# Optimization experiments

Hardware: AMD Instinct MI355X
Metric: run time of the kernel (lower is better)

The kernel has to match this reference:

```python
import jax, jax.numpy as jnp
import numpy as np

N = 100000
E = 1600000
IN_C = 512
OUT_C = 128


def setup_inputs() -> dict:
    key = jax.random.key(0)
    k1, k2, k3, k4 = jax.random.split(key, 4)
    x = jax.random.normal(k1, (N, IN_C), dtype=jnp.float32)
    edge_index = jax.random.randint(k2, (2, E), 0, N, dtype=jnp.int64)
    # GCNConv parameters (glorot weight, zero bias as in PyG defaults)
    scale = jnp.sqrt(6.0 / (IN_C + OUT_C)).astype(jnp.float32)
    W = jax.random.uniform(k3, (IN_C, OUT_C), dtype=jnp.float32, minval=-scale, maxval=scale)
    b = jnp.zeros((OUT_C,), dtype=jnp.float32)
    return {"x": x, "edge_index": edge_index, "W": W, "b": b}


def reference(x, edge_index, W, b):
    n = x.shape[0]
    loops = jnp.arange(n, dtype=edge_index.dtype)
    src = jnp.concatenate([edge_index[0], loops])  # [E+N] message sources
    dst = jnp.concatenate([edge_index[1], loops])  # [E+N] message targets
    # symmetric GCN normalization: deg over targets incl. self-loops
    deg = jax.ops.segment_sum(jnp.ones_like(src, dtype=x.dtype), dst, num_segments=n)
    dinv = jnp.where(deg > 0, jax.lax.rsqrt(deg), 0.0)
    norm = dinv[src] * dinv[dst]  # [E+N]
    h = x @ W  # [N, OUT_C] transform first (in > out)
    msg = h[src] * norm[:, None]  # [E+N, OUT_C]
    out = jax.ops.segment_sum(msg, dst, num_segments=n) + b
    return (out, 0)
```

## Files before the change

### kernel.cpp

```cpp
#include <hip/hip_runtime.h>

#define IN_C 512
#define OUT_C 128
#define NB 128
#define CHUNK 8192

typedef float f32x4 __attribute__((ext_vector_type(4)));
typedef __bf16 bf16x8 __attribute__((ext_vector_type(8)));

static inline int cdiv(int a, int b) { return (a + b - 1) / b; }

__device__ __forceinline__ unsigned short bfbits(__bf16 h) {
  return __builtin_bit_cast(unsigned short, h);
}


__global__ __launch_bounds__(256) void hist_kernel(const int* __restrict__ dst,
                                                   int* __restrict__ table,
                                                   const float* __restrict__ W,
                                                   unsigned short* __restrict__ wfh,
                                                   unsigned short* __restrict__ wfl,
                                                   int nchunks, int E) {
  int c = blockIdx.x;
  int t = threadIdx.x;
  if (c >= nchunks) {
    int i = (c - nchunks) * 256 + t;
    if (i < IN_C * OUT_C) {
      int k = i >> 7;
      int col = i & 127;
      float w = W[i];
      __bf16 hb = (__bf16)w;
      __bf16 lb = (__bf16)(w - (float)hb);
      int ks = k >> 5;
      int lg = (k & 31) >> 3;
      int j = k & 7;
      int cb = col >> 4;
      int lane = lg * 16 + (col & 15);
      size_t idx = ((size_t)(ks * 8 + cb) * 64 + lane) * 8 + j;
      wfh[idx] = bfbits(hb);
      wfl[idx] = bfbits(lb);
    }
    return;
  }
  __shared__ int hcnt[NB];
  if (t < NB) hcnt[t] = 0;
  __syncthreads();
  int base = c * CHUNK;
  int lim = base + CHUNK < E ? base + CHUNK : E;
  for (int e = base + t; e < lim; e += 256) {
    atomicAdd(&hcnt[dst[e] >> 10], 1);
  }
  __syncthreads();
  if (t < NB) table[t * nchunks + c] = hcnt[t];
}

__global__ __launch_bounds__(256) void tscan_kernel(int* __restrict__ table,
                                                    int* __restrict__ bstart,
                                                    int nchunks, int E) {
  __shared__ int sh[256];
  int t = threadIdx.x;
  int total = NB * nchunks;
  int S = (total + 255) / 256;
  int lo = t * S;
  int hi = lo + S; if (hi > total) hi = total;
  int s = 0;
  int i = lo;
  for (; i + 4 <= hi; i += 4)
    s += table[i] + table[i + 1] + table[i + 2] + table[i + 3];
  for (; i < hi; i++) s += table[i];
  sh[t] = s;
  __syncthreads();
  for (int off = 1; off < 256; off <<= 1) {
    int x = sh[t];
    if (t >= off) x += sh[t - off];
    __syncthreads();
    sh[t] = x;
    __syncthreads();
  }
  int run = sh[t] - s;
  for (i = lo; i < hi; i++) {
    int v = table[i];
    table[i] = run;
    run += v;
  }
  __syncthreads();
  for (int b = t; b < NB; b += 256) bstart[b] = table[b * nchunks];
  if (t == 0) bstart[NB] = E;
}

__global__ __launch_bounds__(256) void scat2_kernel(const int* __restrict__ src,
                                                    const int* __restrict__ dst,
                                                    const int* __restrict__ table,
                                                    int* __restrict__ inter,
                                                    int nchunks, int E) {
  __shared__ int cur[NB];
  int t = threadIdx.x;
  int c = blockIdx.x;
  if (t < NB) cur[t] = table[t * nchunks + c];
  __syncthreads();
  int base = c * CHUNK;
  int lim = base + CHUNK < E ? base + CHUNK : E;
  for (int e = base + t; e < lim; e += 256) {
    int d = dst[e];
    int pos = atomicAdd(&cur[d >> 10], 1);
    inter[pos] = (src[e] << 10) | (d & 1023);
  }
}

__global__ __launch_bounds__(256) void bucket_csr_kernel(const int* __restrict__ inter,
                                                         const int* __restrict__ bstart,
                                                         int* __restrict__ offs,
                                                         float* __restrict__ dinv,
                                                         int* __restrict__ csr_src,
                                                         int n, int E, int nbk) {
  __shared__ int dl[1024];
  __shared__ int curs[1024];
  __shared__ int sh[256];
  int t = threadIdx.x;
  int b = blockIdx.x;
  for (int i = t; i < 1024; i += 256) dl[i] = 0;
  __syncthreads();
  int lo = bstart[b], hi = bstart[b + 1];
  for (int e = lo + t; e < hi; e += 256) atomicAdd(&dl[inter[e] & 1023], 1);
  __syncthreads();
  int c[4];
  int s = 0;
#pragma unroll
  for (int j = 0; j < 4; j++) {
    c[j] = dl[t * 4 + j];
    s += c[j];
  }
  sh[t] = s;
  __syncthreads();
  for (int off = 1; off < 256; off <<= 1) {
    int x = sh[t];
    if (t >= off) x += sh[t - off];
    __syncthreads();
    sh[t] = x;
    __syncthreads();
  }
  int run = sh[t] - s + lo;
  int nb0 = b << 10;
#pragma unroll
  for (int j = 0; j < 4; j++) {
    int node = nb0 + t * 4 + j;
    if (node < n) {
      offs[node] = run;
      dinv[node] = rsqrtf((float)c[j] + 1.0f);
    }
    curs[t * 4 + j] = run;
    run += c[j];
  }
  if (b == nbk - 1 && t == 255) offs[n] = E;
  __syncthreads();
  for (int e = lo + t; e < hi; e += 256) {
    int u = inter[e];
    int pos = atomicAdd(&curs[u & 1023], 1);
    csr_src[pos] = u >> 10;
  }
}

__global__ __launch_bounds__(256) void gemm_mfma_kernel(
    const float* __restrict__ x, const unsigned short* __restrict__ wfh,
    const unsigned short* __restrict__ wfl, const float* __restrict__ dinv,
    unsigned short* __restrict__ h, int n) {
  __shared__ float xs[2][4096];

  const int tid = threadIdx.x;
  const int wv = tid >> 6;
  const int lane = tid & 63;
  const int l15 = lane & 15;
  const int lg = lane >> 4;
  const int wr = wv >> 1;
  const int wc = wv & 1;
  const int row0 = blockIdx.x * 128;

  const float* gsrc[4];
#pragma unroll
  for (int i = 0; i < 4; i++) {
    int pslot = i * 256 + tid;
    int row = pslot >> 3;
    int q = pslot & 7;
    int s = q ^ (row & 7);
    int grow = row0 + row;
    if (grow > n - 1) grow = n - 1;
    gsrc[i] = x + (size_t)grow * IN_C + s * 4;
  }

  const unsigned short* bph = wfh + ((size_t)(wc * 4) * 64 + lane) * 8;
  const unsigned short* bpl = wfl + ((size_t)(wc * 4) * 64 + lane) * 8;

  f32x4 acc[4][4];
#pragma unroll
  for (int i = 0; i < 4; i++)
#pragma unroll
    for (int j = 0; j < 4; j++) acc[i][j] = (f32x4)0.0f;

#pragma unroll
  for (int i = 0; i < 4; i++) {
    char* lp = (char*)&xs[0][0] + i * 4096 + wv * 1024;
    __builtin_amdgcn_global_load_lds(
        (const __attribute__((address_space(1))) void*)gsrc[i],
        (__attribute__((address_space(3))) void*)lp, 16, 0, 0);
    gsrc[i] += 32;
  }
  __syncthreads();

  int cur = 0;
  for (int ks = 0; ks < 16; ks++) {
    if (ks < 15) {
#pragma unroll
      for (int i = 0; i < 4; i++) {
        char* lp = (char*)&xs[cur ^ 1][0] + i * 4096 + wv * 1024;
        __builtin_amdgcn_global_load_lds(
            (const __attribute__((address_space(1))) void*)gsrc[i],
            (__attribute__((address_space(3))) void*)lp, 16, 0, 0);
        gsrc[i] += 32;
      }
    }
    bf16x8 bh[4], bl[4];
#pragma unroll
    for (int nt = 0; nt < 4; nt++) {
      bh[nt] = __builtin_bit_cast(bf16x8, *(const uint4*)(bph + (size_t)ks * 4096 + nt * 512));
      bl[nt] = __builtin_bit_cast(bf16x8, *(const uint4*)(bpl + (size_t)ks * 4096 + nt * 512));
    }
    const float* bp = &xs[cur][0];
    bf16x8 ah[4];
#pragma unroll
    for (int rt = 0; rt < 4; rt++) {
      int row = wr * 64 + rt * 16 + l15;
      int r7 = row & 7;
      int s0 = (lg * 2) ^ r7;
      int s1 = (lg * 2 + 1) ^ r7;
      float4 f0 = *(const float4*)(bp + row * 32 + s0 * 4);
      float4 f1 = *(const float4*)(bp + row * 32 + s1 * 4);
      float f[8] = {f0.x, f0.y, f0.z, f0.w, f1.x, f1.y, f1.z, f1.w};
      bf16x8 hh;
#pragma unroll
      for (int j = 0; j < 8; j++) hh[j] = (__bf16)f[j];
      ah[rt] = hh;
    }
#pragma unroll
    for (int rt = 0; rt < 4; rt++)
#pragma unroll
      for (int nt = 0; nt < 4; nt++) {
        acc[rt][nt] = __builtin_amdgcn_mfma_f32_16x16x32_bf16(ah[rt], bh[nt], acc[rt][nt], 0, 0, 0);
        acc[rt][nt] = __builtin_amdgcn_mfma_f32_16x16x32_bf16(ah[rt], bl[nt], acc[rt][nt], 0, 0, 0);
      }
    __syncthreads();
    cur ^= 1;
  }

#pragma unroll
  for (int rt = 0; rt < 4; rt++) {
    int rowbase = row0 + wr * 64 + rt * 16 + lg * 4;
#pragma unroll
    for (int r = 0; r < 4; r++) {
      int row = rowbase + r;
      if (row < n) {
        float di = dinv[row];
#pragma unroll
        for (int nt = 0; nt < 4; nt++) {
          int col = wc * 64 + nt * 16 + l15;
          h[(size_t)row * OUT_C + col] = bfbits((__bf16)(acc[rt][nt][r] * di));
        }
      }
    }
  }
}

__device__ __forceinline__ float bflo(unsigned int u) {
  return __builtin_bit_cast(float, u << 16);
}
__device__ __forceinline__ float bfhi(unsigned int u) {
  return __builtin_bit_cast(float, u & 0xffff0000u);
}

__global__ __launch_bounds__(256) void gather_kernel(const int* __restrict__ offs,
                                                     const int* __restrict__ csr_src,
                                                     const unsigned short* __restrict__ h,
                                                     const float* __restrict__ dinv,
                                                     const float* __restrict__ b,
                                                     float* __restrict__ out,
                                                     int n, int tail) {
  int wid = threadIdx.x >> 6;
  int lane = threadIdx.x & 63;
  int l15 = lane & 15;
  int q = lane >> 4;
  int node = blockIdx.x * 4 + wid;
  if (node >= n) return;

  int start = offs[node];
  int end = offs[node + 1];

  float ax0 = 0, ay0 = 0, ax1 = 0, ay1 = 0, ax2 = 0, ay2 = 0, ax3 = 0, ay3 = 0;

  int e = start + q;
  for (; e + 12 < end; e += 16) {
    int s0 = csr_src[e];
    int s1 = csr_src[e + 4];
    int s2 = csr_src[e + 8];
    int s3 = csr_src[e + 12];
    uint4 u0 = *(const uint4*)(h + (size_t)s0 * OUT_C + l15 * 8);
    uint4 u1 = *(const uint4*)(h + (size_t)s1 * OUT_C + l15 * 8);
    uint4 u2 = *(const uint4*)(h + (size_t)s2 * OUT_C + l15 * 8);
    uint4 u3 = *(const uint4*)(h + (size_t)s3 * OUT_C + l15 * 8);
    ax0 += (bflo(u0.x) + bflo(u1.x)) + (bflo(u2.x) + bflo(u3.x));
    ay0 += (bfhi(u0.x) + bfhi(u1.x)) + (bfhi(u2.x) + bfhi(u3.x));
    ax1 += (bflo(u0.y) + bflo(u1.y)) + (bflo(u2.y) + bflo(u3.y));
    ay1 += (bfhi(u0.y) + bfhi(u1.y)) + (bfhi(u2.y) + bfhi(u3.y));
    ax2 += (bflo(u0.z) + bflo(u1.z)) + (bflo(u2.z) + bflo(u3.z));
    ay2 += (bfhi(u0.z) + bfhi(u1.z)) + (bfhi(u2.z) + bfhi(u3.z));
    ax3 += (bflo(u0.w) + bflo(u1.w)) + (bflo(u2.w) + bflo(u3.w));
    ay3 += (bfhi(u0.w) + bfhi(u1.w)) + (bfhi(u2.w) + bfhi(u3.w));
  }
  for (; e < end; e += 4) {
    int s0 = csr_src[e];
    uint4 u0 = *(const uint4*)(h + (size_t)s0 * OUT_C + l15 * 8);
    ax0 += bflo(u0.x); ay0 += bfhi(u0.x);
    ax1 += bflo(u0.y); ay1 += bfhi(u0.y);
    ax2 += bflo(u0.z); ay2 += bfhi(u0.z);
    ax3 += bflo(u0.w); ay3 += bfhi(u0.w);
  }

#pragma unroll
  for (int mask = 16; mask <= 32; mask <<= 1) {
    ax0 += __shfl_xor(ax0, mask); ay0 += __shfl_xor(ay0, mask);
    ax1 += __shfl_xor(ax1, mask); ay1 += __shfl_xor(ay1, mask);
    ax2 += __shfl_xor(ax2, mask); ay2 += __shfl_xor(ay2, mask);
    ax3 += __shfl_xor(ax3, mask); ay3 += __shfl_xor(ay3, mask);
  }

  float dd = dinv[node];
  uint4 us = *(const uint4*)(h + (size_t)node * OUT_C + l15 * 8);
  ax0 = (ax0 + bflo(us.x)) * dd; ay0 = (ay0 + bfhi(us.x)) * dd;
  ax1 = (ax1 + bflo(us.y)) * dd; ay1 = (ay1 + bfhi(us.y)) * dd;
  ax2 = (ax2 + bflo(us.z)) * dd; ay2 = (ay2 + bfhi(us.z)) * dd;
  ax3 = (ax3 + bflo(us.w)) * dd; ay3 = (ay3 + bfhi(us.w)) * dd;

  if (q == 0) {
    float4 b0 = *(const float4*)(b + l15 * 8);
    float4 b1 = *(const float4*)(b + l15 * 8 + 4);
    float4 o0 = make_float4(ax0 + b0.x, ay0 + b0.y, ax1 + b0.z, ay1 + b0.w);
    float4 o1 = make_float4(ax2 + b1.x, ay2 + b1.y, ax3 + b1.z, ay3 + b1.w);
    float* op = out + (size_t)node * OUT_C + l15 * 8;
    *(float4*)op = o0;
    *(float4*)(op + 4) = o1;
  }

  if (node == 0 && lane == 0) {
    for (int t = 0; t < tail; t++) out[(size_t)n * OUT_C + t] = 0.0f;
  }
}

extern "C" void kernel_launch(void* const* d_in, const int* in_sizes, int n_in,
                              void* d_out, int out_size, void* d_ws, size_t ws_size,
                              hipStream_t stream) {
  const float* x = (const float*)d_in[0];
  const int* ei = (const int*)d_in[1];
  const float* W = (const float*)d_in[2];
  const float* b = (const float*)d_in[3];

  const int n = in_sizes[0] / IN_C;
  const int E = in_sizes[1] / 2;
  const int* src = ei;
  const int* dst = ei + E;
  float* out = (float*)d_out;

  const int nchunks = cdiv(E, CHUNK);
  const int nbk = cdiv(n, 1024);

  size_t p = 0;
  auto alloc = [&](size_t bytes) { size_t o = p; p += (bytes + 255) & ~(size_t)255; return o; };
  char* ws = (char*)d_ws;
  float*          dinv   = (float*)(ws + alloc((size_t)n * 4));
  int*            offs   = (int*)(ws + alloc(((size_t)n + 1) * 4));
  int*            csrsrc = (int*)(ws + alloc((size_t)E * 4));
  int*            bstart = (int*)(ws + alloc((NB + 1) * 4));
  unsigned short* wfh    = (unsigned short*)(ws + alloc((size_t)IN_C * OUT_C * 2));
  unsigned short* wfl    = (unsigned short*)(ws + alloc((size_t)IN_C * OUT_C * 2));
  size_t upos = p;
  int*            inter  = (int*)(ws + upos);
  int*            table  = (int*)(ws + upos + (((size_t)E * 4 + 255) & ~(size_t)255));
  unsigned short* h      = (unsigned short*)(ws + upos);

  hist_kernel<<<nchunks + 256, 256, 0, stream>>>(dst, table, W, wfh, wfl, nchunks, E);
  tscan_kernel<<<1, 256, 0, stream>>>(table, bstart, nchunks, E);
  scat2_kernel<<<nchunks, 256, 0, stream>>>(src, dst, table, inter, nchunks, E);
  bucket_csr_kernel<<<nbk, 256, 0, stream>>>(inter, bstart, offs, dinv, csrsrc, n, E, nbk);
  gemm_mfma_kernel<<<cdiv(n, 128), 256, 0, stream>>>(x, wfh, wfl, dinv, h, n);
  int tail = out_size - n * OUT_C;
  gather_kernel<<<cdiv(n, 4), 256, 0, stream>>>(offs, csrsrc, h, dinv, b, out, n, tail);
}
```

Before: 257.6 us.

## Overlap GEMM tiles with CSR-building kernels and rescale h separately

```diff
diff --git a/kernel.cpp b/kernel.cpp
--- a/kernel.cpp
+++ b/kernel.cpp
@@ -13,7 +13,12 @@
 __device__ __forceinline__ unsigned short bfbits(__bf16 h) {
   return __builtin_bit_cast(unsigned short, h);
 }
-
+__device__ __forceinline__ float bflo(unsigned int u) {
+  return __builtin_bit_cast(float, u << 16);
+}
+__device__ __forceinline__ float bfhi(unsigned int u) {
+  return __builtin_bit_cast(float, u & 0xffff0000u);
+}
 
 __global__ __launch_bounds__(256) void hist_kernel(const int* __restrict__ dst,
                                                    int* __restrict__ table,
@@ -54,9 +59,123 @@
   if (t < NB) table[t * nchunks + c] = hcnt[t];
 }
 
-__global__ __launch_bounds__(256) void tscan_kernel(int* __restrict__ table,
-                                                    int* __restrict__ bstart,
-                                                    int nchunks, int E) {
+__device__ __forceinline__ void gemm_tile(
+    const float* __restrict__ x, const unsigned short* __restrict__ wfh,
+    const unsigned short* __restrict__ wfl, unsigned short* __restrict__ h,
+    int n, int tile) {
+  __shared__ float xs[2][4096];
+
+  const int tid = threadIdx.x;
+  const int wv = tid >> 6;
+  const int lane = tid & 63;
+  const int l15 = lane & 15;
+  const int lg = lane >> 4;
+  const int wr = wv >> 1;
+  const int wc = wv & 1;
+  const int row0 = tile * 128;
+
+  const float* gsrc[4];
+#pragma unroll
+  for (int i = 0; i < 4; i++) {
+    int pslot = i * 256 + tid;
+    int row = pslot >> 3;
+    int q = pslot & 7;
+    int s = q ^ (row & 7);
+    int grow = row0 + row;
+    if (grow > n - 1) grow = n - 1;
+    gsrc[i] = x + (size_t)grow * IN_C + s * 4;
+  }
+
+  const unsigned short* bph = wfh + ((size_t)(wc * 4) * 64 + lane) * 8;
+  const unsigned short* bpl = wfl + ((size_t)(wc * 4) * 64 + lane) * 8;
+
+  f32x4 acc[4][4];
+#pragma unroll
+  for (int i = 0; i < 4; i++)
+#pragma unroll
+    for (int j = 0; j < 4; j++) acc[i][j] = (f32x4)0.0f;
+
+#pragma unroll
+  for (int i = 0; i < 4; i++) {
+    char* lp = (char*)&xs[0][0] + i * 4096 + wv * 1024;
+    __builtin_amdgcn_global_load_lds(
+        (const __attribute__((address_space(1))) void*)gsrc[i],
+        (__attribute__((address_space(3))) void*)lp, 16, 0, 0);
+    gsrc[i] += 32;
+  }
+  __syncthreads();
+
+  int cur = 0;
+  for (int ks = 0; ks < 16; ks++) {
+    if (ks < 15) {
+#pragma unroll
+      for (int i = 0; i < 4; i++) {
+        char* lp = (char*)&xs[cur ^ 1][0] + i * 4096 + wv * 1024;
+        __builtin_amdgcn_global_load_lds(
+            (const __attribute__((address_space(1))) void*)gsrc[i],
+            (__attribute__((address_space(3))) void*)lp, 16, 0, 0);
+        gsrc[i] += 32;
+      }
+    }
+    bf16x8 bh[4], bl[4];
+#pragma unroll
+    for (int nt = 0; nt < 4; nt++) {
+      bh[nt] = __builtin_bit_cast(bf16x8, *(const uint4*)(bph + (size_t)ks * 4096 + nt * 512));
+      bl[nt] = __builtin_bit_cast(bf16x8, *(const uint4*)(bpl + (size_t)ks * 4096 + nt * 512));
+    }
+    const float* bp = &xs[cur][0];
+    bf16x8 ah[4];
+#pragma unroll
+    for (int rt = 0; rt < 4; rt++) {
+      int row = wr * 64 + rt * 16 + l15;
+      int r7 = row & 7;
+      int s0 = (lg * 2) ^ r7;
+      int s1 = (lg * 2 + 1) ^ r7;
+      float4 f0 = *(const float4*)(bp + row * 32 + s0 * 4);
+      float4 f1 = *(const float4*)(bp + row * 32 + s1 * 4);
+      float f[8] = {f0.x, f0.y, f0.z, f0.w, f1.x, f1.y, f1.z, f1.w};
+      bf16x8 hh;
+#pragma unroll
+      for (int j = 0; j < 8; j++) hh[j] = (__bf16)f[j];
+      ah[rt] = hh;
+    }
+#pragma unroll
+    for (int rt = 0; rt < 4; rt++)
+#pragma unroll
+      for (int nt = 0; nt < 4; nt++) {
+        acc[rt][nt] = __builtin_amdgcn_mfma_f32_16x16x32_bf16(ah[rt], bh[nt], acc[rt][nt], 0, 0, 0);
+        acc[rt][nt] = __builtin_amdgcn_mfma_f32_16x16x32_bf16(ah[rt], bl[nt], acc[rt][nt], 0, 0, 0);
+      }
+    __syncthreads();
+    cur ^= 1;
+  }
+
+#pragma unroll
+  for (int rt = 0; rt < 4; rt++) {
+    int rowbase = row0 + wr * 64 + rt * 16 + lg * 4;
+#pragma unroll
+    for (int r = 0; r < 4; r++) {
+      int row = rowbase + r;
+      if (row < n) {
+#pragma unroll
+        for (int nt = 0; nt < 4; nt++) {
+          int col = wc * 64 + nt * 16 + l15;
+          h[(size_t)row * OUT_C + col] = bfbits((__bf16)acc[rt][nt][r]);
+        }
+      }
+    }
+  }
+}
+
+__global__ __launch_bounds__(256) void tscan_gemm_kernel(
+    int* __restrict__ table, int* __restrict__ bstart,
+    const float* __restrict__ x, const unsigned short* __restrict__ wfh,
+    const unsigned short* __restrict__ wfl, unsigned short* __restrict__ h,
+    int nchunks, int E, int n, int tbase) {
+  if (blockIdx.x != 0) {
+    gemm_tile(x, wfh, wfl, h, n, tbase + (int)blockIdx.x - 1);
+    return;
+  }
   __shared__ int sh[256];
   int t = threadIdx.x;
   int total = NB * nchunks;
@@ -71,10 +190,10 @@
   sh[t] = s;
   __syncthreads();
   for (int off = 1; off < 256; off <<= 1) {
-    int x = sh[t];
-    if (t >= off) x += sh[t - off];
+    int x2 = sh[t];
+    if (t >= off) x2 += sh[t - off];
     __syncthreads();
-    sh[t] = x;
+    sh[t] = x2;
     __syncthreads();
   }
   int run = sh[t] - s;
@@ -88,11 +207,16 @@
   if (t == 0) bstart[NB] = E;
 }
 
-__global__ __launch_bounds__(256) void scat2_kernel(const int* __restrict__ src,
-                                                    const int* __restrict__ dst,
-                                                    const int* __restrict__ table,
-                                                    int* __restrict__ inter,
-                                                    int nchunks, int E) {
+__global__ __launch_bounds__(256) void scat2_gemm_kernel(
+    const int* __restrict__ src, const int* __restrict__ dst,
+    const int* __restrict__ table, int* __restrict__ inter,
+    const float* __restrict__ x, const unsigned short* __restrict__ wfh,
+    const unsigned short* __restrict__ wfl, unsigned short* __restrict__ h,
+    int nchunks, int E, int n, int tbase) {
+  if ((int)blockIdx.x >= nchunks) {
+    gemm_tile(x, wfh, wfl, h, n, tbase + (int)blockIdx.x - nchunks);
+    return;
+  }
   __shared__ int cur[NB];
   int t = threadIdx.x;
   int c = blockIdx.x;
@@ -107,12 +231,16 @@
   }
 }
 
-__global__ __launch_bounds__(256) void bucket_csr_kernel(const int* __restrict__ inter,
-                                                         const int* __restrict__ bstart,
-                                                         int* __restrict__ offs,
-                                                         float* __restrict__ dinv,
-                                                         int* __restrict__ csr_src,
-                                                         int n, int E, int nbk) {
+__global__ __launch_bounds__(256) void bucket_gemm_kernel(
+    const int* __restrict__ inter, const int* __restrict__ bstart,
+    int* __restrict__ offs, float* __restrict__ dinv, int* __restrict__ csr_src,
+    const float* __restrict__ x, const unsigned short* __restrict__ wfh,
+    const unsigned short* __restrict__ wfl, unsigned short* __restrict__ h,
+    int n, int E, int nbk, int tbase) {
+  if ((int)blockIdx.x >= nbk) {
+    gemm_tile(x, wfh, wfl, h, n, tbase + (int)blockIdx.x - nbk);
+    return;
+  }
   __shared__ int dl[1024];
   __shared__ int curs[1024];
   __shared__ int sh[256];
@@ -133,10 +261,10 @@
   sh[t] = s;
   __syncthreads();
   for (int off = 1; off < 256; off <<= 1) {
-    int x = sh[t];
-    if (t >= off) x += sh[t - off];
+    int x2 = sh[t];
+    if (t >= off) x2 += sh[t - off];
     __syncthreads();
-    sh[t] = x;
+    sh[t] = x2;
     __syncthreads();
   }
   int run = sh[t] - s + lo;
@@ -160,120 +288,22 @@
   }
 }
 
-__global__ __launch_bounds__(256) void gemm_mfma_kernel(
-    const float* __restrict__ x, const unsigned short* __restrict__ wfh,
-    const unsigned short* __restrict__ wfl, const float* __restrict__ dinv,
-    unsigned short* __restrict__ h, int n) {
-  __shared__ float xs[2][4096];
-
-  const int tid = threadIdx.x;
-  const int wv = tid >> 6;
-  const int lane = tid & 63;
-  const int l15 = lane & 15;
-  const int lg = lane >> 4;
-  const int wr = wv >> 1;
-  const int wc = wv & 1;
-  const int row0 = blockIdx.x * 128;
-
-  const float* gsrc[4];
-#pragma unroll
-  for (int i = 0; i < 4; i++) {
-    int pslot = i * 256 + tid;
-    int row = pslot >> 3;
-    int q = pslot & 7;
-    int s = q ^ (row & 7);
-    int grow = row0 + row;
-    if (grow > n - 1) grow = n - 1;
-    gsrc[i] = x + (size_t)grow * IN_C + s * 4;
-  }
-
-  const unsigned short* bph = wfh + ((size_t)(wc * 4) * 64 + lane) * 8;
-  const unsigned short* bpl = wfl + ((size_t)(wc * 4) * 64 + lane) * 8;
-
-  f32x4 acc[4][4];
-#pragma unroll
-  for (int i = 0; i < 4; i++)
-#pragma unroll
-    for (int j = 0; j < 4; j++) acc[i][j] = (f32x4)0.0f;
-
-#pragma unroll
-  for (int i = 0; i < 4; i++) {
-    char* lp = (char*)&xs[0][0] + i * 4096 + wv * 1024;
-    __builtin_amdgcn_global_load_lds(
-        (const __attribute__((address_space(1))) void*)gsrc[i],
-        (__attribute__((address_space(3))) void*)lp, 16, 0, 0);
-    gsrc[i] += 32;
-  }
-  __syncthreads();
-
-  int cur = 0;
-  for (int ks = 0; ks < 16; ks++) {
-    if (ks < 15) {
-#pragma unroll
-      for (int i = 0; i < 4; i++) {
-        char* lp = (char*)&xs[cur ^ 1][0] + i * 4096 + wv * 1024;
-        __builtin_amdgcn_global_load_lds(
-            (const __attribute__((address_space(1))) void*)gsrc[i],
-            (__attribute__((address_space(3))) void*)lp, 16, 0, 0);
-        gsrc[i] += 32;
-      }
-    }
-    bf16x8 bh[4], bl[4];
-#pragma unroll
-    for (int nt = 0; nt < 4; nt++) {
-      bh[nt] = __builtin_bit_cast(bf16x8, *(const uint4*)(bph + (size_t)ks * 4096 + nt * 512));
-      bl[nt] = __builtin_bit_cast(bf16x8, *(const uint4*)(bpl + (size_t)ks * 4096 + nt * 512));
-    }
-    const float* bp = &xs[cur][0];
-    bf16x8 ah[4];
-#pragma unroll
-    for (int rt = 0; rt < 4; rt++) {
-      int row = wr * 64 + rt * 16 + l15;
-      int r7 = row & 7;
-      int s0 = (lg * 2) ^ r7;
-      int s1 = (lg * 2 + 1) ^ r7;
-      float4 f0 = *(const float4*)(bp + row * 32 + s0 * 4);
-      float4 f1 = *(const float4*)(bp + row * 32 + s1 * 4);
-      float f[8] = {f0.x, f0.y, f0.z, f0.w, f1.x, f1.y, f1.z, f1.w};
-      bf16x8 hh;
-#pragma unroll
-      for (int j = 0; j < 8; j++) hh[j] = (__bf16)f[j];
-      ah[rt] = hh;
-    }
-#pragma unroll
-    for (int rt = 0; rt < 4; rt++)
-#pragma unroll
-      for (int nt = 0; nt < 4; nt++) {
-        acc[rt][nt] = __builtin_amdgcn_mfma_f32_16x16x32_bf16(ah[rt], bh[nt], acc[rt][nt], 0, 0, 0);
-        acc[rt][nt] = __builtin_amdgcn_mfma_f32_16x16x32_bf16(ah[rt], bl[nt], acc[rt][nt], 0, 0, 0);
-      }
-    __syncthreads();
-    cur ^= 1;
-  }
-
-#pragma unroll
-  for (int rt = 0; rt < 4; rt++) {
-    int rowbase = row0 + wr * 64 + rt * 16 + lg * 4;
-#pragma unroll
-    for (int r = 0; r < 4; r++) {
-      int row = rowbase + r;
-      if (row < n) {
-        float di = dinv[row];
-#pragma unroll
-        for (int nt = 0; nt < 4; nt++) {
-          int col = wc * 64 + nt * 16 + l15;
-          h[(size_t)row * OUT_C + col] = bfbits((__bf16)(acc[rt][nt][r] * di));
-        }
-      }
-    }
-  }
-}
-
-__device__ __forceinline__ float bflo(unsigned int u) {
-  return __builtin_bit_cast(float, u << 16);
-}
-__device__ __forceinline__ float bfhi(unsigned int u) {
-  return __builtin_bit_cast(float, u & 0xffff0000u);
+__global__ __launch_bounds__(256) void hscale_kernel(uint4* __restrict__ hw,
+                                                     const float* __restrict__ dinv,
+                                                     int n) {
+  int gid = blockIdx.x * 256 + threadIdx.x;
+  int total = n * 16;
+  if (gid >= total) return;
+  int row = gid >> 4;
+  float d = dinv[row];
+  uint4 u = hw[gid];
+  auto sc = [&](unsigned int v) -> unsigned int {
+    unsigned short lb = bfbits((__bf16)(bflo(v) * d));
+    unsigned short hb = bfbits((__bf16)(bfhi(v) * d));
+    return (unsigned int)lb | ((unsigned int)hb << 16);
+  };
+  u.x = sc(u.x); u.y = sc(u.y); u.z = sc(u.z); u.w = sc(u.w);
+  hw[gid] = u;
 }
 
 __global__ __launch_bounds__(256) void gather_kernel(const int* __restrict__ offs,
@@ -369,6 +399,11 @@
 
   const int nchunks = cdiv(E, CHUNK);
   const int nbk = cdiv(n, 1024);
+  const int ntiles = cdiv(n, 128);
+  int t2 = ntiles < 128 ? ntiles : 128;
+  int rem = ntiles - t2;
+  int t3 = rem < 416 ? rem : 416;
+  int t4 = rem - t3;
 
   size_t p = 0;
   auto alloc = [&](size_t bytes) { size_t o = p; p += (bytes + 255) & ~(size_t)255; return o; };
@@ -379,16 +414,18 @@
   int*            bstart = (int*)(ws + alloc((NB + 1) * 4));
   unsigned short* wfh    = (unsigned short*)(ws + alloc((size_t)IN_C * OUT_C * 2));
   unsigned short* wfl    = (unsigned short*)(ws + alloc((size_t)IN_C * OUT_C * 2));
-  size_t upos = p;
-  int*            inter  = (int*)(ws + upos);
-  int*            table  = (int*)(ws + upos + (((size_t)E * 4 + 255) & ~(size_t)255));
-  unsigned short* h      = (unsigned short*)(ws + upos);
+  unsigned short* h      = (unsigned short*)(ws + alloc((size_t)n * OUT_C * 2));
+  int*            inter  = (int*)(ws + alloc((size_t)E * 4));
+  int*            table  = (int*)(ws + alloc((size_t)NB * nchunks * 4));
 
   hist_kernel<<<nchunks + 256, 256, 0, stream>>>(dst, table, W, wfh, wfl, nchunks, E);
-  tscan_kernel<<<1, 256, 0, stream>>>(table, bstart, nchunks, E);
-  scat2_kernel<<<nchunks, 256, 0, stream>>>(src, dst, table, inter, nchunks, E);
-  bucket_csr_kernel<<<nbk, 256, 0, stream>>>(inter, bstart, offs, dinv, csrsrc, n, E, nbk);
-  gemm_mfma_kernel<<<cdiv(n, 128), 256, 0, stream>>>(x, wfh, wfl, dinv, h, n);
+  tscan_gemm_kernel<<<1 + t2, 256, 0, stream>>>(table, bstart, x, wfh, wfl, h,
+                                                nchunks, E, n, 0);
+  scat2_gemm_kernel<<<nchunks + t3, 256, 0, stream>>>(src, dst, table, inter,
+                                                      x, wfh, wfl, h, nchunks, E, n, t2);
+  bucket_gemm_kernel<<<nbk + t4, 256, 0, stream>>>(inter, bstart, offs, dinv, csrsrc,
+                                                   x, wfh, wfl, h, n, E, nbk, t2 + t3);
+  hscale_kernel<<<cdiv(n * 16, 256), 256, 0, stream>>>((uint4*)h, dinv, n);
   int tail = out_size - n * OUT_C;
   gather_kernel<<<cdiv(n, 4), 256, 0, stream>>>(offs, csrsrc, h, dinv, b, out, n, tail);
 }
```

Measured after the change: 243.3 us (median of 2 runs). -5.5%, faster.
